# Optimization experiments

Hardware: AMD Instinct MI355X
Metric: run time of the kernel (lower is better)

## Reference

```python
import jax, jax.numpy as jnp
import numpy as np


def _aggregate(x, w, k, pad):
    """Involution-style per-pixel local conv.
    x: [N, C, H, W]; w: [N, heads, wc, k*k, H, W] (stride=1, dilation=1, zero pad).
    Returns [N, heads, C, H, W].
    """
    N, C, H, W = x.shape
    heads, wc = w.shape[1], w.shape[2]
    G = C // wc  # channel groups sharing the same per-pixel weights (c % wc)
    xp = jnp.pad(x, ((0, 0), (0, 0), (pad, pad), (pad, pad)))
    # unfold: [N, C, k*k, H, W] via k*k static shifted slices (no dynamic indexing)
    patches = jnp.stack(
        [xp[:, :, i:i + H, j:j + W] for i in range(k) for j in range(k)], axis=2
    )
    p = patches.reshape(N, G, wc, k * k, H, W)
    # out[n, e, g, v, h, w] = sum_k w[n, e, v, k, h, w] * p[n, g, v, k, h, w]
    out = jnp.einsum('nevkhw,ngvkhw->negvhw', w, p)
    return out.reshape(N, heads, C, H, W)


def reference(x, weight1, weight2):
    out1 = _aggregate(x, weight1, 3, 1)  # 3x3 branch, pad=1
    out2 = _aggregate(x, weight2, 5, 2)  # 5x5 branch, pad=2
    # output layout [N, 2, heads, C, H, W] matching the CUDA index arithmetic
    return jnp.stack([out1, out2], axis=1)


def setup_inputs() -> dict:
    key = jax.random.key(0)
    k1, k2, k3 = jax.random.split(key, 3)
    N, C, H, W = 4, 256, 56, 56
    heads, wc = 1, 32
    x = jax.random.normal(k1, (N, C, H, W), dtype=jnp.float32)
    weight1 = jax.random.normal(k2, (N, heads, wc, 9, H, W), dtype=jnp.float32)
    weight2 = jax.random.normal(k3, (N, heads, wc, 25, H, W), dtype=jnp.float32)
    return {"x": x, "weight1": weight1, "weight2": weight2}
```

## Files before the change

### kernel.cpp

```cpp
#include <hip/hip_runtime.h>


#define N_  4
#define C_  256
#define H_  56
#define W_  56
#define HW_ 3136
#define WC_ 32
#define G_  8

__global__ __launch_bounds__(256) void lconv_kernel(
    const float* __restrict__ x,
    const float* __restrict__ w1,
    const float* __restrict__ w2,
    float* __restrict__ out)
{
    const int gid = blockIdx.x * 256 + threadIdx.x;
    const int hw = gid % HW_;
    const int nv = gid / HW_;
    const int v  = nv % WC_;
    const int n  = nv / WC_;
    const int h  = hw / W_;
    const int w  = hw % W_;

    float wt1[9];
    float wt2[25];
    {
        const float* p1 = w1 + (size_t)((n * WC_ + v) * 9) * HW_ + hw;
        #pragma unroll
        for (int p = 0; p < 9; ++p) wt1[p] = p1[p * HW_];
        const float* p2 = w2 + (size_t)((n * WC_ + v) * 25) * HW_ + hw;
        #pragma unroll
        for (int p = 0; p < 25; ++p) wt2[p] = p2[p * HW_];
    }

    float* o1 = out + ((size_t)(n * 2 + 0) * C_ + v) * HW_ + hw;
    float* o2 = out + ((size_t)(n * 2 + 1) * C_ + v) * HW_ + hw;

    for (int g = 0; g < G_; ++g) {
        const int c = g * WC_ + v;
        const float* xp = x + ((size_t)n * C_ + c) * HW_;

        float patch[25];
        #pragma unroll
        for (int di = 0; di < 5; ++di) {
            const int hh = h + di - 2;
            const bool hok = (hh >= 0) & (hh < H_);
            #pragma unroll
            for (int dj = 0; dj < 5; ++dj) {
                const int ww = w + dj - 2;
                const bool ok = hok & (ww >= 0) & (ww < W_);
                patch[di * 5 + dj] = ok ? xp[hh * W_ + ww] : 0.0f;
            }
        }

        float acc1 = 0.0f;
        float acc2 = 0.0f;
        #pragma unroll
        for (int p = 0; p < 25; ++p) acc2 += wt2[p] * patch[p];
        #pragma unroll
        for (int di = 0; di < 3; ++di)
            #pragma unroll
            for (int dj = 0; dj < 3; ++dj)
                acc1 += wt1[di * 3 + dj] * patch[(di + 1) * 5 + (dj + 1)];

        o1[(size_t)g * WC_ * HW_] = acc1;
        o2[(size_t)g * WC_ * HW_] = acc2;
    }
}

extern "C" void kernel_launch(void* const* d_in, const int* in_sizes, int n_in,
                              void* d_out, int out_size, void* d_ws, size_t ws_size,
                              hipStream_t stream) {
    const float* x  = (const float*)d_in[0];
    const float* w1 = (const float*)d_in[1];
    const float* w2 = (const float*)d_in[2];
    float* out = (float*)d_out;

    const int total = N_ * WC_ * HW_;
    dim3 grid(total / 256), block(256);
    hipLaunchKernelGGL(lconv_kernel, grid, block, 0, stream, x, w1, w2, out);
}
```

Before: 119.5 us.

## Compute two adjacent pixels per thread with float2 loads and register-accumulated groups

Each thread now handles two horizontally adjacent output pixels and iterates row-by-row over the 5x5 window, keeping accumulators for all 8 channel groups in registers. Input rows are fetched as three float2 loads shared between both pixels, and weights and outputs use float2 accesses. This cuts per-pixel load instructions and redundant cached input reads, at the cost of higher register pressure and half as many threads.

```diff
diff --git a/kernel.cpp b/kernel.cpp
--- a/kernel.cpp
+++ b/kernel.cpp
@@ -8,6 +8,8 @@
 #define HW_ 3136
 #define WC_ 32
 #define G_  8
+#define W2_ 28
+#define HW2_ 1568
 
 __global__ __launch_bounds__(256) void lconv_kernel(
     const float* __restrict__ x,
@@ -16,56 +18,72 @@
     float* __restrict__ out)
 {
     const int gid = blockIdx.x * 256 + threadIdx.x;
-    const int hw = gid % HW_;
-    const int nv = gid / HW_;
-    const int v  = nv % WC_;
-    const int n  = nv / WC_;
-    const int h  = hw / W_;
-    const int w  = hw % W_;
+    const int hw2 = gid % HW2_;
+    const int nv  = gid / HW2_;
+    const int v   = nv % WC_;
+    const int n   = nv / WC_;
+    const int h   = hw2 / W2_;
+    const int wb  = (hw2 % W2_) * 2;
+    const int hw  = h * W_ + wb;
 
-    float wt1[9];
-    float wt2[25];
-    {
-        const float* p1 = w1 + (size_t)((n * WC_ + v) * 9) * HW_ + hw;
+    const float* w1t = w1 + (size_t)nv * 9  * HW_ + hw;
+    const float* w2t = w2 + (size_t)nv * 25 * HW_ + hw;
+    const float* xb  = x + ((size_t)n * C_ + v) * HW_ + hw;
+
+    float acc1x[G_], acc1y[G_], acc2x[G_], acc2y[G_];
+    #pragma unroll
+    for (int g = 0; g < G_; ++g) { acc1x[g]=0.f; acc1y[g]=0.f; acc2x[g]=0.f; acc2y[g]=0.f; }
+
+    const bool aok = (wb > 0);
+    const bool cok = (wb < W_ - 2);
+
+    #pragma unroll
+    for (int di = 0; di < 5; ++di) {
+        const int hh = h + di - 2;
+        const bool hok = (hh >= 0) && (hh < H_);
+
+        float2 wr2[5];
         #pragma unroll
-        for (int p = 0; p < 9; ++p) wt1[p] = p1[p * HW_];
-        const float* p2 = w2 + (size_t)((n * WC_ + v) * 25) * HW_ + hw;
+        for (int dj = 0; dj < 5; ++dj)
+            wr2[dj] = *(const float2*)(w2t + (size_t)(di * 5 + dj) * HW_);
+        float2 wr1[3];
+        if (di >= 1 && di <= 3) {
+            #pragma unroll
+            for (int dj = 0; dj < 3; ++dj)
+                wr1[dj] = *(const float2*)(w1t + (size_t)((di - 1) * 3 + dj) * HW_);
+        }
+
+        const int rowoff = (di - 2) * W_;
         #pragma unroll
-        for (int p = 0; p < 25; ++p) wt2[p] = p2[p * HW_];
+        for (int g = 0; g < G_; ++g) {
+            const float* xr = xb + (size_t)g * WC_ * HW_ + rowoff;
+            const float2 z = make_float2(0.f, 0.f);
+            float2 xa = (hok && aok) ? *(const float2*)(xr - 2) : z;
+            float2 xm =  hok         ? *(const float2*)(xr)     : z;
+            float2 xc = (hok && cok) ? *(const float2*)(xr + 2) : z;
+            const float xw[6] = {xa.x, xa.y, xm.x, xm.y, xc.x, xc.y};
+
+            #pragma unroll
+            for (int dj = 0; dj < 5; ++dj) {
+                acc2x[g] += wr2[dj].x * xw[dj];
+                acc2y[g] += wr2[dj].y * xw[dj + 1];
+            }
+            if (di >= 1 && di <= 3) {
+                #pragma unroll
+                for (int dj = 0; dj < 3; ++dj) {
+                    acc1x[g] += wr1[dj].x * xw[dj + 1];
+                    acc1y[g] += wr1[dj].y * xw[dj + 2];
+                }
+            }
+        }
     }
 
     float* o1 = out + ((size_t)(n * 2 + 0) * C_ + v) * HW_ + hw;
     float* o2 = out + ((size_t)(n * 2 + 1) * C_ + v) * HW_ + hw;
-
+    #pragma unroll
     for (int g = 0; g < G_; ++g) {
-        const int c = g * WC_ + v;
-        const float* xp = x + ((size_t)n * C_ + c) * HW_;
-
-        float patch[25];
-        #pragma unroll
-        for (int di = 0; di < 5; ++di) {
-            const int hh = h + di - 2;
-            const bool hok = (hh >= 0) & (hh < H_);
-            #pragma unroll
-            for (int dj = 0; dj < 5; ++dj) {
-                const int ww = w + dj - 2;
-                const bool ok = hok & (ww >= 0) & (ww < W_);
-                patch[di * 5 + dj] = ok ? xp[hh * W_ + ww] : 0.0f;
-            }
-        }
-
-        float acc1 = 0.0f;
-        float acc2 = 0.0f;
-        #pragma unroll
-        for (int p = 0; p < 25; ++p) acc2 += wt2[p] * patch[p];
-        #pragma unroll
-        for (int di = 0; di < 3; ++di)
-            #pragma unroll
-            for (int dj = 0; dj < 3; ++dj)
-                acc1 += wt1[di * 3 + dj] * patch[(di + 1) * 5 + (dj + 1)];
-
-        o1[(size_t)g * WC_ * HW_] = acc1;
-        o2[(size_t)g * WC_ * HW_] = acc2;
+        *(float2*)(o1 + (size_t)g * WC_ * HW_) = make_float2(acc1x[g], acc1y[g]);
+        *(float2*)(o2 + (size_t)g * WC_ * HW_) = make_float2(acc2x[g], acc2y[g]);
     }
 }
 
@@ -77,7 +95,7 @@
     const float* w2 = (const float*)d_in[2];
     float* out = (float*)d_out;
 
-    const int total = N_ * WC_ * HW_;
+    const int total = N_ * WC_ * HW2_;
     dim3 grid(total / 256), block(256);
     hipLaunchKernelGGL(lconv_kernel, grid, block, 0, stream, x, w1, w2, out);
 }
```

Result: slower. 135.6 us (+13.4%).
